# Kernel tuning notes

Measured on AMD Instinct MI355X. Metric: run time of the kernel, lower is better.

## Reference

```python
import jax, jax.numpy as jnp
import numpy as np

N_PRED = 29
F_DIM = 8192
H1 = 256
H2 = 128


def setup_inputs() -> dict:
    key = jax.random.key(0)
    ks = jax.random.split(key, 7)
    features = jax.random.normal(ks[0], (4096, F_DIM), dtype=jnp.float32)
    # Stacked per-predicate MLP weights (PyTorch Linear init scale ~ 1/sqrt(fan_in))
    W1 = jax.random.normal(ks[1], (N_PRED, F_DIM, H1), dtype=jnp.float32) / np.sqrt(F_DIM)
    b1 = jax.random.normal(ks[2], (N_PRED, H1), dtype=jnp.float32) / np.sqrt(F_DIM)
    W2 = jax.random.normal(ks[3], (N_PRED, H1, H2), dtype=jnp.float32) / np.sqrt(H1)
    b2 = jax.random.normal(ks[4], (N_PRED, H2), dtype=jnp.float32) / np.sqrt(H1)
    W3 = jax.random.normal(ks[5], (N_PRED, H2), dtype=jnp.float32) / np.sqrt(H2)
    b3 = jax.random.normal(ks[6], (N_PRED,), dtype=jnp.float32) / np.sqrt(H2)
    return {"features": features, "W1": W1, "b1": b1, "W2": W2, "b2": b2, "W3": W3, "b3": b3}


def reference(features, W1, b1, W2, b2, W3, b3):
    # 29 parallel heads as one batched (grouped) GEMM chain; dropout = identity (eval).
    h1 = jax.nn.relu(jnp.einsum('bf,pfh->bph', features, W1) + b1[None])   # [B, P, H1]
    h2 = jax.nn.relu(jnp.einsum('bph,phk->bpk', h1, W2) + b2[None])        # [B, P, H2]
    logits = jnp.einsum('bpk,pk->bp', h2, W3) + b3[None]                   # [B, P]
    return jax.nn.sigmoid(logits)
```

## Files before the change

### kernel.cpp

```cpp
#include <hip/hip_runtime.h>
#include <hip/hip_bf16.h>

typedef __attribute__((ext_vector_type(8))) short short8_t;
typedef __attribute__((ext_vector_type(8))) __bf16 bf16x8;
typedef __attribute__((ext_vector_type(4))) float f32x4;

__device__ __forceinline__ void gload16(const void* g, void* l) {
  __builtin_amdgcn_global_load_lds(
      (const __attribute__((address_space(1))) void*)g,
      (__attribute__((address_space(3))) void*)l, 16, 0, 0);
}

__device__ __forceinline__ unsigned short f2bf(float f) {
  __hip_bfloat16 h = __float2bfloat16(f);
  return __builtin_bit_cast(unsigned short, h);
}

#define BARRIER() asm volatile("s_barrier" ::: "memory")


__global__ void k_cvt_feat(const float* __restrict__ in, unsigned short* __restrict__ out) {
  const size_t N = (size_t)4096 * 8192;
  size_t i = ((size_t)blockIdx.x * 256 + threadIdx.x) * 4;
  const size_t stride = (size_t)gridDim.x * 256 * 4;
  for (; i < N; i += stride) {
    float4 v = *(const float4*)(in + i);
    ushort4 o;
    o.x = f2bf(v.x); o.y = f2bf(v.y); o.z = f2bf(v.z); o.w = f2bf(v.w);
    *(ushort4*)(out + i) = o;
  }
}

__global__ void k_cvt_w1(const float* __restrict__ W1, unsigned short* __restrict__ out, int p0) {
  __shared__ unsigned short t[64][66];
  const int p = p0 + blockIdx.z;
  const float* src = W1 + (size_t)p * 8192 * 256;
  unsigned short* dst = out + (size_t)blockIdx.z * 256 * 8192;
  const int f0 = blockIdx.x * 64, h0 = blockIdx.y * 64;
#pragma unroll
  for (int i = 0; i < 16; ++i) {
    int tt = i * 256 + threadIdx.x;
    int r = tt >> 6, c = tt & 63;
    t[r][c] = f2bf(src[(size_t)(f0 + r) * 256 + h0 + c]);
  }
  __syncthreads();
#pragma unroll
  for (int i = 0; i < 16; ++i) {
    int tt = i * 256 + threadIdx.x;
    int r = tt >> 6, c = tt & 63;
    dst[(size_t)(h0 + r) * 8192 + f0 + c] = t[c][r];
  }
}

__global__ void k_cvt_w2(const float* __restrict__ W2, unsigned short* __restrict__ out) {
  const int p = blockIdx.x;
  const float* src = W2 + (size_t)p * 256 * 128;
  unsigned short* dst = out + (size_t)p * 128 * 256;
  for (int tt = threadIdx.x; tt < 128 * 256; tt += 256) {
    int j = tt >> 8, h = tt & 255;
    dst[tt] = f2bf(src[(size_t)h * 128 + j]);
  }
}

__global__ __launch_bounds__(512, 2) void k_gemm1(
    const unsigned short* __restrict__ A,
    const unsigned short* __restrict__ Bt,
    const float* __restrict__ b1,
    unsigned short* __restrict__ h1,
    int p0) {
  __shared__ __align__(16) unsigned short S[65536];

  const int tid = threadIdx.x;
  const int lane = tid & 63;
  const int wave = tid >> 6;
  const int wm = wave >> 2;
  const int wn = wave & 3;

  const int nwg = gridDim.x * gridDim.y;
  const int orig = blockIdx.y * gridDim.x + blockIdx.x;
  const int q = nwg >> 3, r_ = nwg & 7;
  const int xcd = orig & 7, idx = orig >> 3;
  const int wg = (xcd < r_ ? xcd * (q + 1) : r_ * (q + 1) + (xcd - r_) * q) + idx;
  const int mx = wg & 15;
  const int z = wg >> 4;
  const int p = p0 + z;
  const int m0 = mx * 256;

  const unsigned short* Ab = A + (size_t)m0 * 8192;
  const unsigned short* Bb = Bt + (size_t)z * 256 * 8192;

  int e0 = tid, r0 = e0 >> 3, u0 = (e0 & 7) ^ (r0 & 7);
  int e1 = 512 + tid, r1e = e1 >> 3, u1 = (e1 & 7) ^ (r1e & 7);
  const size_t s0 = (size_t)r0 * 8192 + u0 * 8;
  const size_t s1 = (size_t)r1e * 8192 + u1 * 8;
  const int ld0 = (wave * 64) * 8;
  const int ld1 = (512 + wave * 64) * 8;

  auto stage = [&](int buf, int isB, int h, int T) {
    const unsigned short* gb = (isB ? Bb : Ab) + (size_t)h * 128 * 8192 + (size_t)T * 64;
    unsigned short* lb = S + buf * 32768 + isB * 16384 + h * 8192;
    gload16(gb + s0, lb + ld0);
    gload16(gb + s1, lb + ld1);
  };

  const int l15 = lane & 15, ks = lane >> 4;

  auto rdA = [&](int buf, int mi, int x) {
    int R = wm * 128 + mi * 16 + l15;
    int pu = (x * 4 + ks) ^ (R & 7);
    return __builtin_bit_cast(bf16x8, *(const short8_t*)(S + buf * 32768 + R * 64 + pu * 8));
  };
  auto rdB = [&](int buf, int nj, int x) {
    int R = wn * 64 + nj * 16 + l15;
    int pu = (x * 4 + ks) ^ (R & 7);
    return __builtin_bit_cast(bf16x8, *(const short8_t*)(S + buf * 32768 + 16384 + R * 64 + pu * 8));
  };

  f32x4 acc[8][4] = {};
  const int NT = 8192 / 64;

  auto kstep = [&](int t, int pf1, int pf4, int vm) {
    const int c = t & 1, nx = c ^ 1;
    bf16x8 aF[4][2], bL[2][2], bH[2][2];
#pragma unroll
    for (int mi = 0; mi < 4; ++mi) { aF[mi][0] = rdA(c, mi, 0); aF[mi][1] = rdA(c, mi, 1); }
#pragma unroll
    for (int nj = 0; nj < 2; ++nj) { bL[nj][0] = rdB(c, nj, 0); bL[nj][1] = rdB(c, nj, 1); }
    if (pf1) stage(nx, 0, 1, t + 1);
    BARRIER();
    __builtin_amdgcn_s_setprio(1);
#pragma unroll
    for (int mi = 0; mi < 4; ++mi)
#pragma unroll
      for (int nj = 0; nj < 2; ++nj) {
        acc[mi][nj] = __builtin_amdgcn_mfma_f32_16x16x32_bf16(aF[mi][0], bL[nj][0], acc[mi][nj], 0, 0, 0);
        acc[mi][nj] = __builtin_amdgcn_mfma_f32_16x16x32_bf16(aF[mi][1], bL[nj][1], acc[mi][nj], 0, 0, 0);
      }
    __builtin_amdgcn_s_setprio(0);
    BARRIER();
#pragma unroll
    for (int nj = 0; nj < 2; ++nj) { bH[nj][0] = rdB(c, nj + 2, 0); bH[nj][1] = rdB(c, nj + 2, 1); }
    if (pf1) stage(nx, 1, 0, t + 1);
    BARRIER();
    __builtin_amdgcn_s_setprio(1);
#pragma unroll
    for (int mi = 0; mi < 4; ++mi)
#pragma unroll
      for (int nj = 0; nj < 2; ++nj) {
        acc[mi][nj + 2] = __builtin_amdgcn_mfma_f32_16x16x32_bf16(aF[mi][0], bH[nj][0], acc[mi][nj + 2], 0, 0, 0);
        acc[mi][nj + 2] = __builtin_amdgcn_mfma_f32_16x16x32_bf16(aF[mi][1], bH[nj][1], acc[mi][nj + 2], 0, 0, 0);
      }
    __builtin_amdgcn_s_setprio(0);
    BARRIER();
#pragma unroll
    for (int mi = 0; mi < 4; ++mi) { aF[mi][0] = rdA(c, mi + 4, 0); aF[mi][1] = rdA(c, mi + 4, 1); }
    if (pf1) stage(nx, 1, 1, t + 1);
    BARRIER();
    __builtin_amdgcn_s_setprio(1);
#pragma unroll
    for (int mi = 0; mi < 4; ++mi)
#pragma unroll
      for (int nj = 0; nj < 2; ++nj) {
        acc[mi + 4][nj] = __builtin_amdgcn_mfma_f32_16x16x32_bf16(aF[mi][0], bL[nj][0], acc[mi + 4][nj], 0, 0, 0);
        acc[mi + 4][nj] = __builtin_amdgcn_mfma_f32_16x16x32_bf16(aF[mi][1], bL[nj][1], acc[mi + 4][nj], 0, 0, 0);
      }
    __builtin_amdgcn_s_setprio(0);
    BARRIER();
    if (pf4) stage(c, 0, 0, t + 2);
    if (vm == 2)      asm volatile("s_waitcnt vmcnt(2)" ::: "memory");
    else if (vm == 0) asm volatile("s_waitcnt vmcnt(0)" ::: "memory");
    BARRIER();
    __builtin_amdgcn_s_setprio(1);
#pragma unroll
    for (int mi = 0; mi < 4; ++mi)
#pragma unroll
      for (int nj = 0; nj < 2; ++nj) {
        acc[mi + 4][nj + 2] = __builtin_amdgcn_mfma_f32_16x16x32_bf16(aF[mi][0], bH[nj][0], acc[mi + 4][nj + 2], 0, 0, 0);
        acc[mi + 4][nj + 2] = __builtin_amdgcn_mfma_f32_16x16x32_bf16(aF[mi][1], bH[nj][1], acc[mi + 4][nj + 2], 0, 0, 0);
      }
    __builtin_amdgcn_s_setprio(0);
    BARRIER();
  };

  stage(0, 0, 0, 0); stage(0, 0, 1, 0); stage(0, 1, 0, 0); stage(0, 1, 1, 0);
  stage(1, 0, 0, 1);
  asm volatile("s_waitcnt vmcnt(2)" ::: "memory");
  BARRIER();

  for (int t = 0; t < NT - 2; ++t) kstep(t, 1, 1, 2);
  kstep(NT - 2, 1, 0, 0);
  kstep(NT - 1, 0, 0, -1);

  const int rg = lane >> 4;
#pragma unroll
  for (int nj = 0; nj < 4; ++nj) {
    const int col = wn * 64 + nj * 16 + l15;
    const float bb = b1[p * 256 + col];
#pragma unroll
    for (int mi = 0; mi < 8; ++mi) {
      const int rbase = m0 + wm * 128 + mi * 16 + rg * 4;
#pragma unroll
      for (int rr = 0; rr < 4; ++rr) {
        float v = acc[mi][nj][rr] + bb;
        v = v > 0.f ? v : 0.f;
        h1[((size_t)p * 4096 + rbase + rr) * 256 + col] = f2bf(v);
      }
    }
  }
}

__global__ __launch_bounds__(256, 2) void k_gemm23(
    const unsigned short* __restrict__ h1,
    const unsigned short* __restrict__ W2t,
    const float* __restrict__ b2,
    const float* __restrict__ W3,
    const float* __restrict__ b3,
    float* __restrict__ out) {
  __shared__ __align__(16) unsigned short lds_a[128 * 64];
  __shared__ __align__(16) unsigned short lds_b[128 * 64];
  const int tid = threadIdx.x;
  const int lane = tid & 63;
  const int wave = tid >> 6;
  const int m0 = blockIdx.x * 128;
  const int p = blockIdx.y;

  const unsigned short* Ab = h1 + ((size_t)p * 4096 + m0) * 256;
  const unsigned short* Bb = W2t + (size_t)p * 128 * 256;

  f32x4 acc[2][8] = {};

  for (int k0 = 0; k0 < 256; k0 += 64) {
    __syncthreads();
#pragma unroll
    for (int i = 0; i < 4; ++i) {
      int t = i * 256 + tid;
      int r = t >> 3;
      int uu = (t & 7) ^ (r & 7);
      gload16(Ab + (size_t)r * 256 + k0 + uu * 8, &lds_a[(i * 256 + wave * 64) * 8]);
      gload16(Bb + (size_t)r * 256 + k0 + uu * 8, &lds_b[(i * 256 + wave * 64) * 8]);
    }
    __syncthreads();
#pragma unroll
    for (int kk = 0; kk < 64; kk += 32) {
      const int ku = (kk >> 3) + (lane >> 4);
      bf16x8 af[2], bfv[8];
#pragma unroll
      for (int mi = 0; mi < 2; ++mi) {
        int row = wave * 32 + mi * 16 + (lane & 15);
        int u = ku ^ (row & 7);
        af[mi] = __builtin_bit_cast(bf16x8, *(const short8_t*)&lds_a[row * 64 + u * 8]);
      }
#pragma unroll
      for (int nj = 0; nj < 8; ++nj) {
        int row = nj * 16 + (lane & 15);
        int u = ku ^ (row & 7);
        bfv[nj] = __builtin_bit_cast(bf16x8, *(const short8_t*)&lds_b[row * 64 + u * 8]);
      }
#pragma unroll
      for (int mi = 0; mi < 2; ++mi)
#pragma unroll
        for (int nj = 0; nj < 8; ++nj)
          acc[mi][nj] = __builtin_amdgcn_mfma_f32_16x16x32_bf16(af[mi], bfv[nj], acc[mi][nj], 0, 0, 0);
    }
  }

  float b2v[8], w3v[8];
  const int c16 = lane & 15;
#pragma unroll
  for (int nj = 0; nj < 8; ++nj) {
    int c = nj * 16 + c16;
    b2v[nj] = b2[p * 128 + c];
    w3v[nj] = W3[p * 128 + c];
  }
  const float b3p = b3[p];
#pragma unroll
  for (int mi = 0; mi < 2; ++mi) {
#pragma unroll
    for (int r = 0; r < 4; ++r) {
      float s = 0.f;
#pragma unroll
      for (int nj = 0; nj < 8; ++nj) {
        float v = acc[mi][nj][r] + b2v[nj];
        v = v > 0.f ? v : 0.f;
        s += v * w3v[nj];
      }
      s += __shfl_xor(s, 1);
      s += __shfl_xor(s, 2);
      s += __shfl_xor(s, 4);
      s += __shfl_xor(s, 8);
      if ((lane & 15) == 0) {
        int m = m0 + wave * 32 + mi * 16 + (lane >> 4) * 4 + r;
        float logit = s + b3p;
        out[(size_t)m * 29 + p] = 1.f / (1.f + __expf(-logit));
      }
    }
  }
}

extern "C" void kernel_launch(void* const* d_in, const int* in_sizes, int n_in,
                              void* d_out, int out_size, void* d_ws, size_t ws_size,
                              hipStream_t stream) {
  const float* features = (const float*)d_in[0];
  const float* W1 = (const float*)d_in[1];
  const float* b1 = (const float*)d_in[2];
  const float* W2 = (const float*)d_in[3];
  const float* b2 = (const float*)d_in[4];
  const float* W3 = (const float*)d_in[5];
  const float* b3 = (const float*)d_in[6];
  float* out = (float*)d_out;

  char* ws = (char*)d_ws;
  const size_t featB = (size_t)4096 * 8192 * 2;
  const size_t h1B   = (size_t)29 * 4096 * 256 * 2;
  const size_t w2B   = (size_t)29 * 128 * 256 * 2;
  const size_t w1pp  = (size_t)256 * 8192 * 2;

  unsigned short* featbf = (unsigned short*)ws;
  unsigned short* h1bf   = (unsigned short*)(ws + featB);
  unsigned short* w2t    = (unsigned short*)(ws + featB + h1B);
  unsigned short* w1t    = (unsigned short*)(ws + featB + h1B + w2B);

  size_t base = featB + h1B + w2B;
  size_t rem = (ws_size > base) ? (ws_size - base) : 0;
  int CH = (int)(rem / w1pp);
  if (CH > 29) CH = 29;
  if (CH < 1) CH = 1;

  k_cvt_feat<<<2048, 256, 0, stream>>>(features, featbf);
  k_cvt_w2<<<29, 256, 0, stream>>>(W2, w2t);

  for (int p0 = 0; p0 < 29; p0 += CH) {
    int c = (29 - p0) < CH ? (29 - p0) : CH;
    k_cvt_w1<<<dim3(128, 4, c), 256, 0, stream>>>(W1, w1t, p0);
    k_gemm1<<<dim3(16, c), 512, 0, stream>>>(featbf, w1t, b1, h1bf, p0);
  }

  k_gemm23<<<dim3(32, 29), 256, 0, stream>>>(h1bf, w2t, b2, W3, b3, out);
}
```

Measured before the change: 614.1 us.

## Restructure GEMM1 wave tiling into quadrant layout with two-stage prefetch schedule

```diff
diff --git a/kernel.cpp b/kernel.cpp
--- a/kernel.cpp
+++ b/kernel.cpp
@@ -73,16 +73,17 @@
   const int tid = threadIdx.x;
   const int lane = tid & 63;
   const int wave = tid >> 6;
-  const int wm = wave >> 2;
-  const int wn = wave & 3;
-
-  const int nwg = gridDim.x * gridDim.y;
+  const int sr = (wave >> 2) * 64;
+  const int sc = (wave & 3) * 32;
+
+  const int nz = gridDim.y;
+  const int nwg = gridDim.x * nz;
   const int orig = blockIdx.y * gridDim.x + blockIdx.x;
   const int q = nwg >> 3, r_ = nwg & 7;
   const int xcd = orig & 7, idx = orig >> 3;
   const int wg = (xcd < r_ ? xcd * (q + 1) : r_ * (q + 1) + (xcd - r_) * q) + idx;
-  const int mx = wg & 15;
-  const int z = wg >> 4;
+  const int mx = wg / nz;
+  const int z = wg % nz;
   const int p = p0 + z;
   const int m0 = mx * 256;
 
@@ -105,108 +106,112 @@
 
   const int l15 = lane & 15, ks = lane >> 4;
 
-  auto rdA = [&](int buf, int mi, int x) {
-    int R = wm * 128 + mi * 16 + l15;
+  auto rdA = [&](int buf, int h, int mi, int x) {
+    int R = sr + mi * 16 + l15;
     int pu = (x * 4 + ks) ^ (R & 7);
-    return __builtin_bit_cast(bf16x8, *(const short8_t*)(S + buf * 32768 + R * 64 + pu * 8));
+    return __builtin_bit_cast(bf16x8, *(const short8_t*)(S + buf * 32768 + h * 8192 + R * 64 + pu * 8));
   };
-  auto rdB = [&](int buf, int nj, int x) {
-    int R = wn * 64 + nj * 16 + l15;
+  auto rdB = [&](int buf, int v, int nj, int x) {
+    int R = sc + nj * 16 + l15;
     int pu = (x * 4 + ks) ^ (R & 7);
-    return __builtin_bit_cast(bf16x8, *(const short8_t*)(S + buf * 32768 + 16384 + R * 64 + pu * 8));
+    return __builtin_bit_cast(bf16x8, *(const short8_t*)(S + buf * 32768 + 16384 + v * 8192 + R * 64 + pu * 8));
   };
 
-  f32x4 acc[8][4] = {};
+  f32x4 acc[4][4][2] = {};
   const int NT = 8192 / 64;
 
-  auto kstep = [&](int t, int pf1, int pf4, int vm) {
+  auto kstep = [&](int t, int pf, int vm1, int vm4) {
     const int c = t & 1, nx = c ^ 1;
-    bf16x8 aF[4][2], bL[2][2], bH[2][2];
-#pragma unroll
-    for (int mi = 0; mi < 4; ++mi) { aF[mi][0] = rdA(c, mi, 0); aF[mi][1] = rdA(c, mi, 1); }
-#pragma unroll
-    for (int nj = 0; nj < 2; ++nj) { bL[nj][0] = rdB(c, nj, 0); bL[nj][1] = rdB(c, nj, 1); }
-    if (pf1) stage(nx, 0, 1, t + 1);
+    bf16x8 a[4][2], bl[2][2], bh[2][2];
+#pragma unroll
+    for (int mi = 0; mi < 4; ++mi) { a[mi][0] = rdA(c, 0, mi, 0); a[mi][1] = rdA(c, 0, mi, 1); }
+#pragma unroll
+    for (int nj = 0; nj < 2; ++nj) { bl[nj][0] = rdB(c, 0, nj, 0); bl[nj][1] = rdB(c, 0, nj, 1); }
+    if (pf) { stage(nx, 0, 0, t + 1); stage(nx, 1, 0, t + 1); }
     BARRIER();
     __builtin_amdgcn_s_setprio(1);
 #pragma unroll
     for (int mi = 0; mi < 4; ++mi)
 #pragma unroll
       for (int nj = 0; nj < 2; ++nj) {
-        acc[mi][nj] = __builtin_amdgcn_mfma_f32_16x16x32_bf16(aF[mi][0], bL[nj][0], acc[mi][nj], 0, 0, 0);
-        acc[mi][nj] = __builtin_amdgcn_mfma_f32_16x16x32_bf16(aF[mi][1], bL[nj][1], acc[mi][nj], 0, 0, 0);
+        acc[0][mi][nj] = __builtin_amdgcn_mfma_f32_16x16x32_bf16(a[mi][0], bl[nj][0], acc[0][mi][nj], 0, 0, 0);
+        acc[0][mi][nj] = __builtin_amdgcn_mfma_f32_16x16x32_bf16(a[mi][1], bl[nj][1], acc[0][mi][nj], 0, 0, 0);
       }
     __builtin_amdgcn_s_setprio(0);
-    BARRIER();
-#pragma unroll
-    for (int nj = 0; nj < 2; ++nj) { bH[nj][0] = rdB(c, nj + 2, 0); bH[nj][1] = rdB(c, nj + 2, 1); }
-    if (pf1) stage(nx, 1, 0, t + 1);
+    if (vm1 == 4)      asm volatile("s_waitcnt vmcnt(4)" ::: "memory");
+    else if (vm1 == 0) asm volatile("s_waitcnt vmcnt(0)" ::: "memory");
+    BARRIER();
+#pragma unroll
+    for (int nj = 0; nj < 2; ++nj) { bh[nj][0] = rdB(c, 1, nj, 0); bh[nj][1] = rdB(c, 1, nj, 1); }
     BARRIER();
     __builtin_amdgcn_s_setprio(1);
 #pragma unroll
     for (int mi = 0; mi < 4; ++mi)
 #pragma unroll
       for (int nj = 0; nj < 2; ++nj) {
-        acc[mi][nj + 2] = __builtin_amdgcn_mfma_f32_16x16x32_bf16(aF[mi][0], bH[nj][0], acc[mi][nj + 2], 0, 0, 0);
-        acc[mi][nj + 2] = __builtin_amdgcn_mfma_f32_16x16x32_bf16(aF[mi][1], bH[nj][1], acc[mi][nj + 2], 0, 0, 0);
+        acc[1][mi][nj] = __builtin_amdgcn_mfma_f32_16x16x32_bf16(a[mi][0], bh[nj][0], acc[1][mi][nj], 0, 0, 0);
+        acc[1][mi][nj] = __builtin_amdgcn_mfma_f32_16x16x32_bf16(a[mi][1], bh[nj][1], acc[1][mi][nj], 0, 0, 0);
       }
     __builtin_amdgcn_s_setprio(0);
     BARRIER();
 #pragma unroll
-    for (int mi = 0; mi < 4; ++mi) { aF[mi][0] = rdA(c, mi + 4, 0); aF[mi][1] = rdA(c, mi + 4, 1); }
-    if (pf1) stage(nx, 1, 1, t + 1);
+    for (int mi = 0; mi < 4; ++mi) { a[mi][0] = rdA(c, 1, mi, 0); a[mi][1] = rdA(c, 1, mi, 1); }
+    if (pf) { stage(nx, 1, 1, t + 1); stage(nx, 0, 1, t + 1); }
     BARRIER();
     __builtin_amdgcn_s_setprio(1);
 #pragma unroll
     for (int mi = 0; mi < 4; ++mi)
 #pragma unroll
       for (int nj = 0; nj < 2; ++nj) {
-        acc[mi + 4][nj] = __builtin_amdgcn_mfma_f32_16x16x32_bf16(aF[mi][0], bL[nj][0], acc[mi + 4][nj], 0, 0, 0);
-        acc[mi + 4][nj] = __builtin_amdgcn_mfma_f32_16x16x32_bf16(aF[mi][1], bL[nj][1], acc[mi + 4][nj], 0, 0, 0);
+        acc[2][mi][nj] = __builtin_amdgcn_mfma_f32_16x16x32_bf16(a[mi][0], bl[nj][0], acc[2][mi][nj], 0, 0, 0);
+        acc[2][mi][nj] = __builtin_amdgcn_mfma_f32_16x16x32_bf16(a[mi][1], bl[nj][1], acc[2][mi][nj], 0, 0, 0);
       }
     __builtin_amdgcn_s_setprio(0);
     BARRIER();
-    if (pf4) stage(c, 0, 0, t + 2);
-    if (vm == 2)      asm volatile("s_waitcnt vmcnt(2)" ::: "memory");
-    else if (vm == 0) asm volatile("s_waitcnt vmcnt(0)" ::: "memory");
-    BARRIER();
     __builtin_amdgcn_s_setprio(1);
 #pragma unroll
     for (int mi = 0; mi < 4; ++mi)
 #pragma unroll
       for (int nj = 0; nj < 2; ++nj) {
-        acc[mi + 4][nj + 2] = __builtin_amdgcn_mfma_f32_16x16x32_bf16(aF[mi][0], bH[nj][0], acc[mi + 4][nj + 2], 0, 0, 0);
-        acc[mi + 4][nj + 2] = __builtin_amdgcn_mfma_f32_16x16x32_bf16(aF[mi][1], bH[nj][1], acc[mi + 4][nj + 2], 0, 0, 0);
+        acc[3][mi][nj] = __builtin_amdgcn_mfma_f32_16x16x32_bf16(a[mi][0], bh[nj][0], acc[3][mi][nj], 0, 0, 0);
+        acc[3][mi][nj] = __builtin_amdgcn_mfma_f32_16x16x32_bf16(a[mi][1], bh[nj][1], acc[3][mi][nj], 0, 0, 0);
       }
     __builtin_amdgcn_s_setprio(0);
+    if (vm4 == 4)      asm volatile("s_waitcnt vmcnt(4)" ::: "memory");
+    else if (vm4 == 0) asm volatile("s_waitcnt vmcnt(0)" ::: "memory");
     BARRIER();
   };
 
-  stage(0, 0, 0, 0); stage(0, 0, 1, 0); stage(0, 1, 0, 0); stage(0, 1, 1, 0);
-  stage(1, 0, 0, 1);
-  asm volatile("s_waitcnt vmcnt(2)" ::: "memory");
+  stage(0, 0, 0, 0); stage(0, 1, 0, 0);
+  stage(0, 1, 1, 0); stage(0, 0, 1, 0);
+  asm volatile("s_waitcnt vmcnt(4)" ::: "memory");
   BARRIER();
 
-  for (int t = 0; t < NT - 2; ++t) kstep(t, 1, 1, 2);
-  kstep(NT - 2, 1, 0, 0);
+  for (int t = 0; t < NT - 1; ++t) kstep(t, 1, 4, 4);
   kstep(NT - 1, 0, 0, -1);
 
   const int rg = lane >> 4;
 #pragma unroll
-  for (int nj = 0; nj < 4; ++nj) {
-    const int col = wn * 64 + nj * 16 + l15;
-    const float bb = b1[p * 256 + col];
-#pragma unroll
-    for (int mi = 0; mi < 8; ++mi) {
-      const int rbase = m0 + wm * 128 + mi * 16 + rg * 4;
-#pragma unroll
-      for (int rr = 0; rr < 4; ++rr) {
-        float v = acc[mi][nj][rr] + bb;
-        v = v > 0.f ? v : 0.f;
-        h1[((size_t)p * 4096 + rbase + rr) * 256 + col] = f2bf(v);
+  for (int qh = 0; qh < 2; ++qh)
+#pragma unroll
+    for (int qv = 0; qv < 2; ++qv) {
+      const int qq = qh * 2 + qv;
+#pragma unroll
+      for (int nj = 0; nj < 2; ++nj) {
+        const int col = qv * 128 + sc + nj * 16 + l15;
+        const float bb = b1[p * 256 + col];
+#pragma unroll
+        for (int mi = 0; mi < 4; ++mi) {
+          const int rbase = m0 + qh * 128 + sr + mi * 16 + rg * 4;
+#pragma unroll
+          for (int rr = 0; rr < 4; ++rr) {
+            float v = acc[qq][mi][nj][rr] + bb;
+            v = v > 0.f ? v : 0.f;
+            h1[((size_t)p * 4096 + rbase + rr) * 256 + col] = f2bf(v);
+          }
+        }
       }
     }
-  }
 }
 
 __global__ __launch_bounds__(256, 2) void k_gemm23(
```

After: 563.2 us. 8.3% less time.
